# Kernel tuning notes

Measured on AMD Instinct MI355X. Metric: run time of the kernel, lower is better.

## Reference

```python
import jax, jax.numpy as jnp
import numpy as np

D_MODEL = 1024
D_FFN = 2048
N_EXPERTS = 8
TOP_K = 2
B, S = 2, 2048
LN_EPS = 1e-5


def setup_inputs() -> dict:
    key = jax.random.key(0)
    ks = jax.random.split(key, 6)
    scale = 0.02
    x = jax.random.normal(ks[0], (B, S, D_MODEL), dtype=jnp.float32)
    w_router = jax.random.normal(ks[1], (N_EXPERTS, D_MODEL), dtype=jnp.float32) * scale
    w_gate = jax.random.normal(ks[2], (N_EXPERTS, D_FFN, D_MODEL), dtype=jnp.float32) * scale
    w_up = jax.random.normal(ks[3], (N_EXPERTS, D_FFN, D_MODEL), dtype=jnp.float32) * scale
    w_down = jax.random.normal(ks[4], (N_EXPERTS, D_MODEL, D_FFN), dtype=jnp.float32) * scale
    ln_gamma = jnp.ones((D_MODEL,), dtype=jnp.float32)
    ln_beta = jnp.zeros((D_MODEL,), dtype=jnp.float32)
    return {"x": x, "w_router": w_router, "w_gate": w_gate, "w_up": w_up,
            "w_down": w_down, "ln_gamma": ln_gamma, "ln_beta": ln_beta}


def reference(x, w_router, w_gate, w_up, w_down, ln_gamma, ln_beta):
    # Router: top-k logits, softmax over selected k (matches MoERouter)
    logits = jnp.einsum('bsd,ed->bse', x, w_router)            # [B,S,E]
    top_vals, top_idx = jax.lax.top_k(logits, TOP_K)           # [B,S,k]
    rw = jax.nn.softmax(top_vals, axis=-1)                     # [B,S,k]

    # Dense per-expert SwiGLU over ALL tokens (faithful to the looped original:
    # sum over k of mask*weight*expert(x) == gather of per-expert outputs).
    gate = jnp.einsum('bsd,efd->ebsf', x, w_gate)              # [E,B,S,F]
    up = jnp.einsum('bsd,efd->ebsf', x, w_up)                  # [E,B,S,F]
    h = jax.nn.silu(gate) * up                                 # SwiGLU hidden
    y = jnp.einsum('ebsf,edf->bsed', h, w_down)                # [B,S,E,D]

    # Gather the k selected experts per token and combine with routing weights
    sel = jnp.take_along_axis(y, top_idx[..., None], axis=2)   # [B,S,k,D]
    out = jnp.sum(rw[..., None] * sel, axis=2)                 # [B,S,D]

    # LayerNorm (eps=1e-5, elementwise affine)
    mu = jnp.mean(out, axis=-1, keepdims=True)
    var = jnp.mean(jnp.square(out - mu), axis=-1, keepdims=True)
    out = (out - mu) * jax.lax.rsqrt(var + LN_EPS)
    return out * ln_gamma + ln_beta
```

## Files before the change

### kernel.cpp

```cpp
#include <hip/hip_runtime.h>


#define D_MODEL 1024
#define D_FFN   2048
#define N_EXP   8
#define TOKENS  4096
#define LISTCAP 4096
#define ROWS_PAD 8320
#define W_ELEM  16777216u

typedef __bf16 bf16x8 __attribute__((ext_vector_type(8)));
typedef float  f32x4  __attribute__((ext_vector_type(4)));

__device__ __forceinline__ ushort f2bf(float f) {
  union { float f; unsigned u; } v; v.f = f;
  unsigned u = v.u;
  u += 0x7fffu + ((u >> 16) & 1u);
  return (ushort)(u >> 16);
}
__device__ __forceinline__ float bf2f(ushort h) {
  union { unsigned u; float f; } v; v.u = ((unsigned)h) << 16; return v.f;
}
__device__ __forceinline__ void gl2lds16(const ushort* g, ushort* l) {
  __builtin_amdgcn_global_load_lds(
      (const __attribute__((address_space(1))) unsigned int*)g,
      (__attribute__((address_space(3))) unsigned int*)l, 16, 0, 0);
}


__global__ __launch_bounds__(256) void router_a_kernel(
    const float* __restrict__ x, const float* __restrict__ wr,
    ushort* __restrict__ xb, int* __restrict__ eids, float* __restrict__ wts)
{
  const int token = blockIdx.x * 4 + (threadIdx.x >> 6);
  const int lane  = threadIdx.x & 63;
  const float* xr = x + (size_t)token * D_MODEL + lane * 16;

  float xv[16];
  #pragma unroll
  for (int j = 0; j < 16; ++j) xv[j] = xr[j];

  ushort* xbr = xb + (size_t)token * D_MODEL + lane * 16;
  #pragma unroll
  for (int half = 0; half < 2; ++half) {
    ushort u8[8];
    #pragma unroll
    for (int j = 0; j < 8; ++j) u8[j] = f2bf(xv[half * 8 + j]);
    *(uint4*)(xbr + half * 8) = *(uint4*)u8;
  }

  float logit[N_EXP];
  #pragma unroll
  for (int e = 0; e < N_EXP; ++e) {
    const float* w = wr + e * D_MODEL + lane * 16;
    float p = 0.f;
    #pragma unroll
    for (int j = 0; j < 16; ++j) p += xv[j] * w[j];
    #pragma unroll
    for (int o = 32; o > 0; o >>= 1) p += __shfl_xor(p, o, 64);
    logit[e] = p;
  }

  if (lane == 0) {
    float v0 = -1e30f, v1 = -1e30f; int i0 = 0, i1 = 0;
    #pragma unroll
    for (int e = 0; e < N_EXP; ++e) {
      float v = logit[e];
      if (v > v0)      { v1 = v0; i1 = i0; v0 = v; i0 = e; }
      else if (v > v1) { v1 = v; i1 = e; }
    }
    float t  = expf(v1 - v0);
    eids[token] = i0 | (i1 << 8);
    wts[token * 2]     = 1.f / (1.f + t);
    wts[token * 2 + 1] = t   / (1.f + t);
  }
}

__global__ __launch_bounds__(1024) void build_lists_kernel(
    const int* __restrict__ eids, int* __restrict__ counts,
    int* __restrict__ tok_list, int* __restrict__ slots)
{
  const int e = blockIdx.x;
  const int t = threadIdx.x;

  int my_k[4];
  int c = 0;
  #pragma unroll
  for (int i = 0; i < 4; ++i) {
    int tok = t + i * 1024;
    int p  = eids[tok];
    int e0 = p & 0xff, e1 = (p >> 8) & 0xff;
    my_k[i] = (e0 == e) ? 0 : (e1 == e) ? 1 : -1;
    c += (my_k[i] >= 0) ? 1 : 0;
  }

  const int wave = t >> 6, lane = t & 63;
  int v = c;
  #pragma unroll
  for (int o = 1; o < 64; o <<= 1) {
    int n = __shfl_up(v, o, 64);
    if (lane >= o) v += n;
  }

  __shared__ int wsum[16];
  __shared__ int wbase[16];
  if (lane == 63) wsum[wave] = v;
  __syncthreads();
  if (t == 0) {
    int s = 0;
    #pragma unroll
    for (int w = 0; w < 16; ++w) { wbase[w] = s; s += wsum[w]; }
    counts[e] = s;
  }
  __syncthreads();

  int pos = wbase[wave] + v - c;
  #pragma unroll
  for (int i = 0; i < 4; ++i) {
    int tok = t + i * 1024;
    if (my_k[i] >= 0) {
      tok_list[e * LISTCAP + pos] = tok;
      slots[tok * 2 + my_k[i]] = e * LISTCAP + pos;
      pos++;
    }
  }
}

__global__ __launch_bounds__(256) void convert3_kernel(
    const float* __restrict__ wg, const float* __restrict__ wu,
    const float* __restrict__ wd, ushort* __restrict__ dstBase)
{
  const int bid = blockIdx.x;
  const int arr = bid >> 13;
  const float* src = (arr == 0) ? wg : (arr == 1) ? wu : wd;
  ushort* dst = dstBase + (size_t)arr * W_ELEM;
  const size_t base = (((size_t)(bid & 8191)) * 256 + threadIdx.x) * 8;
  float4 a = *(const float4*)(src + base);
  float4 b = *(const float4*)(src + base + 4);
  ushort u8[8] = {f2bf(a.x), f2bf(a.y), f2bf(a.z), f2bf(a.w),
                  f2bf(b.x), f2bf(b.y), f2bf(b.z), f2bf(b.w)};
  *(uint4*)(dst + base) = *(uint4*)u8;
}

__global__ __launch_bounds__(256, 3) void gateup3_kernel(
    const ushort* __restrict__ xb, const ushort* __restrict__ WgB,
    const ushort* __restrict__ WuB, const int* __restrict__ counts,
    const int* __restrict__ tok_list, ushort* __restrict__ H)
{
  const int e  = blockIdx.z;
  const int Ne = counts[e];
  const int m0 = blockIdx.y * 128;
  if (m0 >= Ne) return;
  const int n0 = blockIdx.x * 64;

  int rowoff = 0;
  for (int j = 0; j < e; ++j) rowoff += counts[j];

  __shared__ ushort As[128 * 64];
  __shared__ ushort Bg[64 * 64];
  __shared__ ushort Bu[64 * 64];
  __shared__ int tok_s[128];

  const int tid = threadIdx.x;
  if (tid < 128) {
    int i = m0 + tid;
    tok_s[tid] = tok_list[e * LISTCAP + (i < Ne ? i : Ne - 1)];
  }
  __syncthreads();

  const int wave = tid >> 6;
  const int lane = tid & 63;
  const int rsub = lane >> 3;
  const int cchk = lane & 7;
  const int co   = (cchk ^ rsub) << 3;

  const ushort* aSrc[4];
  #pragma unroll
  for (int i = 0; i < 4; ++i)
    aSrc[i] = xb + (size_t)tok_s[wave * 32 + i * 8 + rsub] * D_MODEL + co;
  const ushort* gS = WgB + ((size_t)e * D_FFN + n0 + wave * 16 + rsub) * D_MODEL + co;
  const ushort* uS = WuB + ((size_t)e * D_FFN + n0 + wave * 16 + rsub) * D_MODEL + co;
  ushort* aD = &As[(wave * 32) * 64];
  ushort* gD = &Bg[(wave * 16) * 64];
  ushort* uD = &Bu[(wave * 16) * 64];

  const int wm   = (wave >> 1) * 64;
  const int wn   = (wave & 1) * 32;
  const int lrow = lane & 15;
  const int lq   = lane >> 4;

  f32x4 accg[4][2], accu[4][2];
  #pragma unroll
  for (int i = 0; i < 4; ++i)
    #pragma unroll
    for (int j = 0; j < 2; ++j) {
      accg[i][j] = f32x4{0.f, 0.f, 0.f, 0.f};
      accu[i][j] = f32x4{0.f, 0.f, 0.f, 0.f};
    }

  for (int k0 = 0; k0 < D_MODEL; k0 += 64) {
    #pragma unroll
    for (int i = 0; i < 4; ++i) {
      gl2lds16(aSrc[i], aD + i * 8 * 64);
      aSrc[i] += 64;
    }
    #pragma unroll
    for (int i = 0; i < 2; ++i) {
      gl2lds16(gS + (size_t)i * 8 * D_MODEL, gD + i * 8 * 64);
      gl2lds16(uS + (size_t)i * 8 * D_MODEL, uD + i * 8 * 64);
    }
    gS += 64; uS += 64;
    __syncthreads();

    #pragma unroll
    for (int kk = 0; kk < 2; ++kk) {
      const int c = kk * 4 + lq;
      bf16x8 af[4], bgf[2], buf[2];
      #pragma unroll
      for (int mi = 0; mi < 4; ++mi) {
        int r = wm + mi * 16 + lrow;
        af[mi] = *(const bf16x8*)&As[r * 64 + ((c ^ (r & 7)) << 3)];
      }
      #pragma unroll
      for (int ni = 0; ni < 2; ++ni) {
        int r = wn + ni * 16 + lrow;
        int off = r * 64 + ((c ^ (r & 7)) << 3);
        bgf[ni] = *(const bf16x8*)&Bg[off];
        buf[ni] = *(const bf16x8*)&Bu[off];
      }
      #pragma unroll
      for (int mi = 0; mi < 4; ++mi)
        #pragma unroll
        for (int ni = 0; ni < 2; ++ni) {
          accg[mi][ni] = __builtin_amdgcn_mfma_f32_16x16x32_bf16(af[mi], bgf[ni], accg[mi][ni], 0, 0, 0);
          accu[mi][ni] = __builtin_amdgcn_mfma_f32_16x16x32_bf16(af[mi], buf[ni], accu[mi][ni], 0, 0, 0);
        }
    }
    __syncthreads();
  }

  const int rowbase = rowoff + m0;
  #pragma unroll
  for (int mi = 0; mi < 4; ++mi)
    #pragma unroll
    for (int r4 = 0; r4 < 4; ++r4) {
      int m = wm + mi * 16 + lq * 4 + r4;
      if (m0 + m < Ne) {
        ushort* hr = H + (size_t)(rowbase + m) * D_FFN + n0 + wn + lrow;
        #pragma unroll
        for (int ni = 0; ni < 2; ++ni) {
          float g = accg[mi][ni][r4];
          float u = accu[mi][ni][r4];
          float h = g / (1.f + __expf(-g)) * u;
          hr[ni * 16] = f2bf(h);
        }
      }
    }
}

__global__ __launch_bounds__(256, 3) void down3_kernel(
    const ushort* __restrict__ H, const ushort* __restrict__ WdB,
    const int* __restrict__ counts, ushort* __restrict__ Y)
{
  const int e  = blockIdx.z;
  const int Ne = counts[e];
  const int m0 = blockIdx.y * 128;
  if (m0 >= Ne) return;
  const int n0 = blockIdx.x * 128;

  int rowoff = 0;
  for (int j = 0; j < e; ++j) rowoff += counts[j];
  const int rowbase = rowoff + m0;

  __shared__ ushort As[128 * 64];
  __shared__ ushort Bd[128 * 64];

  const int tid  = threadIdx.x;
  const int wave = tid >> 6;
  const int lane = tid & 63;
  const int rsub = lane >> 3;
  const int cchk = lane & 7;
  const int co   = (cchk ^ rsub) << 3;

  const ushort* aS = H   + (size_t)(rowbase + wave * 32 + rsub) * D_FFN + co;
  const ushort* bS = WdB + (size_t)(e * D_MODEL + n0 + wave * 32 + rsub) * D_FFN + co;
  ushort* aD = &As[(wave * 32) * 64];
  ushort* bD = &Bd[(wave * 32) * 64];

  const int wm   = (wave >> 1) * 64;
  const int wn   = (wave & 1) * 64;
  const int lrow = lane & 15;
  const int lq   = lane >> 4;

  f32x4 acc[4][4];
  #pragma unroll
  for (int i = 0; i < 4; ++i)
    #pragma unroll
    for (int j = 0; j < 4; ++j) acc[i][j] = f32x4{0.f, 0.f, 0.f, 0.f};

  for (int k0 = 0; k0 < D_FFN; k0 += 64) {
    #pragma unroll
    for (int i = 0; i < 4; ++i) {
      gl2lds16(aS + (size_t)i * 8 * D_FFN, aD + i * 8 * 64);
      gl2lds16(bS + (size_t)i * 8 * D_FFN, bD + i * 8 * 64);
    }
    aS += 64; bS += 64;
    __syncthreads();

    #pragma unroll
    for (int kk = 0; kk < 2; ++kk) {
      const int c = kk * 4 + lq;
      bf16x8 af[4], bf[4];
      #pragma unroll
      for (int mi = 0; mi < 4; ++mi) {
        int r = wm + mi * 16 + lrow;
        af[mi] = *(const bf16x8*)&As[r * 64 + ((c ^ (r & 7)) << 3)];
      }
      #pragma unroll
      for (int ni = 0; ni < 4; ++ni) {
        int r = wn + ni * 16 + lrow;
        bf[ni] = *(const bf16x8*)&Bd[r * 64 + ((c ^ (r & 7)) << 3)];
      }
      #pragma unroll
      for (int mi = 0; mi < 4; ++mi)
        #pragma unroll
        for (int ni = 0; ni < 4; ++ni)
          acc[mi][ni] = __builtin_amdgcn_mfma_f32_16x16x32_bf16(af[mi], bf[ni], acc[mi][ni], 0, 0, 0);
    }
    __syncthreads();
  }

  #pragma unroll
  for (int mi = 0; mi < 4; ++mi)
    #pragma unroll
    for (int r4 = 0; r4 < 4; ++r4) {
      int m = wm + mi * 16 + lq * 4 + r4;
      if (m0 + m < Ne) {
        ushort* yr = Y + (size_t)(rowbase + m) * D_MODEL + n0 + wn + lrow;
        #pragma unroll
        for (int ni = 0; ni < 4; ++ni)
          yr[ni * 16] = f2bf(acc[mi][ni][r4]);
      }
    }
}

__global__ __launch_bounds__(256) void combine_ln3_kernel(
    const ushort* __restrict__ Y, const int* __restrict__ slots,
    const float* __restrict__ wts, const int* __restrict__ counts,
    const float* __restrict__ gamma, const float* __restrict__ beta,
    float* __restrict__ out)
{
  const int token = blockIdx.x;
  const int t = threadIdx.x;

  __shared__ int offs_s[N_EXP];
  if (t == 0) {
    int s = 0;
    #pragma unroll
    for (int j = 0; j < N_EXP; ++j) { offs_s[j] = s; s += counts[j]; }
  }
  __syncthreads();

  const int s0 = slots[token * 2], s1 = slots[token * 2 + 1];
  const float w0 = wts[token * 2], w1 = wts[token * 2 + 1];
  const int r0 = offs_s[s0 >> 12] + (s0 & (LISTCAP - 1));
  const int r1 = offs_s[s1 >> 12] + (s1 & (LISTCAP - 1));

  ushort4 a = *(const ushort4*)(Y + (size_t)r0 * D_MODEL + t * 4);
  ushort4 b = *(const ushort4*)(Y + (size_t)r1 * D_MODEL + t * 4);
  float4 v;
  v.x = w0 * bf2f(a.x) + w1 * bf2f(b.x);
  v.y = w0 * bf2f(a.y) + w1 * bf2f(b.y);
  v.z = w0 * bf2f(a.z) + w1 * bf2f(b.z);
  v.w = w0 * bf2f(a.w) + w1 * bf2f(b.w);

  float s = v.x + v.y + v.z + v.w;
  #pragma unroll
  for (int o = 32; o > 0; o >>= 1) s += __shfl_xor(s, o, 64);
  __shared__ float red[4];
  const int wave = t >> 6, lane = t & 63;
  if (lane == 0) red[wave] = s;
  __syncthreads();
  float mean = (red[0] + red[1] + red[2] + red[3]) * (1.f / D_MODEL);

  float dx = v.x - mean, dy = v.y - mean, dz = v.z - mean, dw = v.w - mean;
  float ss = dx * dx + dy * dy + dz * dz + dw * dw;
  #pragma unroll
  for (int o = 32; o > 0; o >>= 1) ss += __shfl_xor(ss, o, 64);
  __syncthreads();
  if (lane == 0) red[wave] = ss;
  __syncthreads();
  float var = (red[0] + red[1] + red[2] + red[3]) * (1.f / D_MODEL);
  float rs  = rsqrtf(var + 1e-5f);

  float4 g = ((const float4*)gamma)[t];
  float4 bb = ((const float4*)beta)[t];
  float4 o4;
  o4.x = dx * rs * g.x + bb.x;
  o4.y = dy * rs * g.y + bb.y;
  o4.z = dz * rs * g.z + bb.z;
  o4.w = dw * rs * g.w + bb.w;
  ((float4*)(out + (size_t)token * D_MODEL))[t] = o4;
}

__global__ __launch_bounds__(64) void router_kernel(
    const float* __restrict__ x, const float* __restrict__ wr,
    ushort* __restrict__ xb, int* __restrict__ counts,
    int* __restrict__ tok_list, float* __restrict__ wt_list)
{
  const int token = blockIdx.x;
  const int lane  = threadIdx.x;
  const float* xr = x + (size_t)token * D_MODEL;
  float xv[16];
  #pragma unroll
  for (int j = 0; j < 16; ++j) xv[j] = xr[j * 64 + lane];
  ushort* xbr = xb + (size_t)token * D_MODEL;
  #pragma unroll
  for (int j = 0; j < 16; ++j) xbr[j * 64 + lane] = f2bf(xv[j]);
  float logit[N_EXP];
  #pragma unroll
  for (int e = 0; e < N_EXP; ++e) {
    const float* w = wr + e * D_MODEL;
    float p = 0.f;
    #pragma unroll
    for (int j = 0; j < 16; ++j) p += xv[j] * w[j * 64 + lane];
    #pragma unroll
    for (int o = 32; o > 0; o >>= 1) p += __shfl_xor(p, o, 64);
    logit[e] = p;
  }
  if (lane == 0) {
    float v0 = -1e30f, v1 = -1e30f; int i0 = 0, i1 = 0;
    #pragma unroll
    for (int e = 0; e < N_EXP; ++e) {
      float v = logit[e];
      if (v > v0)      { v1 = v0; i1 = i0; v0 = v; i0 = e; }
      else if (v > v1) { v1 = v; i1 = e; }
    }
    float t  = expf(v1 - v0);
    float w0 = 1.f / (1.f + t);
    float w1 = t   / (1.f + t);
    int p0 = atomicAdd(&counts[i0], 1);
    tok_list[i0 * LISTCAP + p0] = token;
    wt_list[i0 * LISTCAP + p0] = w0;
    int p1 = atomicAdd(&counts[i1], 1);
    tok_list[i1 * LISTCAP + p1] = token;
    wt_list[i1 * LISTCAP + p1] = w1;
  }
}

__global__ void prefix_kernel(const int* __restrict__ counts, int* __restrict__ offsets)
{
  if (threadIdx.x == 0 && blockIdx.x == 0) {
    int s = 0;
    for (int e = 0; e < N_EXP; ++e) { offsets[e] = s; s += counts[e]; }
  }
}

__global__ __launch_bounds__(256, 2) void gateup_kernel(
    const ushort* __restrict__ xb, const float* __restrict__ wg,
    const float* __restrict__ wu, const int* __restrict__ counts,
    const int* __restrict__ offsets, const int* __restrict__ tok_list,
    ushort* __restrict__ H)
{
  const int e  = blockIdx.z;
  const int Ne = counts[e];
  const int m0 = blockIdx.y * 128;
  if (m0 >= Ne) return;
  const int n0 = blockIdx.x * 128;
  __shared__ ushort As[128][80];
  __shared__ ushort Bg[128][80];
  __shared__ ushort Bu[128][80];
  __shared__ int tok_s[128];
  const int tid = threadIdx.x;
  if (tid < 128) {
    int i = m0 + tid;
    tok_s[tid] = tok_list[e * LISTCAP + (i < Ne ? i : 0)];
  }
  __syncthreads();
  const int wave = tid >> 6;
  const int lane = tid & 63;
  const int wm   = (wave >> 1) * 64;
  const int wn   = (wave & 1) * 64;
  const int lrow = lane & 15;
  const int lk   = (lane >> 4) * 8;
  f32x4 accg[4][4], accu[4][4];
  #pragma unroll
  for (int i = 0; i < 4; ++i)
    #pragma unroll
    for (int j = 0; j < 4; ++j) {
      accg[i][j] = f32x4{0.f, 0.f, 0.f, 0.f};
      accu[i][j] = f32x4{0.f, 0.f, 0.f, 0.f};
    }
  const size_t wbase = ((size_t)e * D_FFN + n0) * D_MODEL;
  for (int k0 = 0; k0 < D_MODEL; k0 += 64) {
    #pragma unroll
    for (int r = 0; r < 4; ++r) {
      int idx = tid + r * 256;
      int row = idx >> 3;
      int c8  = (idx & 7) * 8;
      const ushort* src = xb + (size_t)tok_s[row] * D_MODEL + k0 + c8;
      *(uint4*)(&As[row][c8]) = *(const uint4*)src;
    }
    #pragma unroll
    for (int r = 0; r < 8; ++r) {
      int idx = tid + r * 256;
      int row = idx >> 4;
      int c4  = (idx & 15) * 4;
      const size_t off = wbase + (size_t)row * D_MODEL + k0 + c4;
      const float4 g = *(const float4*)(wg + off);
      const float4 u = *(const float4*)(wu + off);
      ushort4 gb; gb.x = f2bf(g.x); gb.y = f2bf(g.y); gb.z = f2bf(g.z); gb.w = f2bf(g.w);
      ushort4 ub; ub.x = f2bf(u.x); ub.y = f2bf(u.y); ub.z = f2bf(u.z); ub.w = f2bf(u.w);
      *(ushort4*)(&Bg[row][c4]) = gb;
      *(ushort4*)(&Bu[row][c4]) = ub;
    }
    __syncthreads();
    #pragma unroll
    for (int kk = 0; kk < 64; kk += 32) {
      bf16x8 af[4], bgf[4], buf[4];
      #pragma unroll
      for (int mi = 0; mi < 4; ++mi)
        af[mi] = *(const bf16x8*)(&As[wm + mi * 16 + lrow][kk + lk]);
      #pragma unroll
      for (int ni = 0; ni < 4; ++ni) {
        bgf[ni] = *(const bf16x8*)(&Bg[wn + ni * 16 + lrow][kk + lk]);
        buf[ni] = *(const bf16x8*)(&Bu[wn + ni * 16 + lrow][kk + lk]);
      }
      #pragma unroll
      for (int mi = 0; mi < 4; ++mi)
        #pragma unroll
        for (int ni = 0; ni < 4; ++ni) {
          accg[mi][ni] = __builtin_amdgcn_mfma_f32_16x16x32_bf16(af[mi], bgf[ni], accg[mi][ni], 0, 0, 0);
          accu[mi][ni] = __builtin_amdgcn_mfma_f32_16x16x32_bf16(af[mi], buf[ni], accu[mi][ni], 0, 0, 0);
        }
    }
    __syncthreads();
  }
  const int row_base = offsets[e] + m0;
  #pragma unroll
  for (int mi = 0; mi < 4; ++mi)
    #pragma unroll
    for (int ni = 0; ni < 4; ++ni)
      #pragma unroll
      for (int r4 = 0; r4 < 4; ++r4) {
        int m = wm + mi * 16 + (lane >> 4) * 4 + r4;
        if (m0 + m < Ne) {
          int n = wn + ni * 16 + (lane & 15);
          float g = accg[mi][ni][r4];
          float u = accu[mi][ni][r4];
          float h = g / (1.f + __expf(-g)) * u;
          H[(size_t)(row_base + m) * D_FFN + (n0 + n)] = f2bf(h);
        }
      }
}

__global__ __launch_bounds__(256, 2) void down_kernel(
    const ushort* __restrict__ H, const float* __restrict__ wd,
    const int* __restrict__ counts, const int* __restrict__ offsets,
    const int* __restrict__ tok_list, const float* __restrict__ wt_list,
    float* __restrict__ out)
{
  const int e  = blockIdx.z;
  const int Ne = counts[e];
  const int m0 = blockIdx.y * 128;
  if (m0 >= Ne) return;
  const int n0 = blockIdx.x * 128;
  __shared__ ushort As[128][80];
  __shared__ ushort Bd[128][80];
  __shared__ int   tok_s[128];
  __shared__ float wt_s[128];
  const int tid = threadIdx.x;
  if (tid < 128) {
    int i  = m0 + tid;
    int ok = (i < Ne);
    tok_s[tid] = tok_list[e * LISTCAP + (ok ? i : 0)];
    wt_s[tid]  = ok ? wt_list[e * LISTCAP + i] : 0.f;
  }
  __syncthreads();
  const int wave = tid >> 6;
  const int lane = tid & 63;
  const int wm   = (wave >> 1) * 64;
  const int wn   = (wave & 1) * 64;
  const int lrow = lane & 15;
  const int lk   = (lane >> 4) * 8;
  const int row_base = offsets[e] + m0;
  f32x4 acc[4][4];
  #pragma unroll
  for (int i = 0; i < 4; ++i)
    #pragma unroll
    for (int j = 0; j < 4; ++j) acc[i][j] = f32x4{0.f, 0.f, 0.f, 0.f};
  const size_t wdbase = ((size_t)e * D_MODEL + n0) * D_FFN;
  for (int k0 = 0; k0 < D_FFN; k0 += 64) {
    #pragma unroll
    for (int r = 0; r < 4; ++r) {
      int idx = tid + r * 256;
      int row = idx >> 3;
      int c8  = (idx & 7) * 8;
      const ushort* src = H + (size_t)(row_base + row) * D_FFN + k0 + c8;
      *(uint4*)(&As[row][c8]) = *(const uint4*)src;
    }
    #pragma unroll
    for (int r = 0; r < 8; ++r) {
      int idx = tid + r * 256;
      int row = idx >> 4;
      int c4  = (idx & 15) * 4;
      const float4 d = *(const float4*)(wd + wdbase + (size_t)row * D_FFN + k0 + c4);
      ushort4 db; db.x = f2bf(d.x); db.y = f2bf(d.y); db.z = f2bf(d.z); db.w = f2bf(d.w);
      *(ushort4*)(&Bd[row][c4]) = db;
    }
    __syncthreads();
    #pragma unroll
    for (int kk = 0; kk < 64; kk += 32) {
      bf16x8 af[4], bdf[4];
      #pragma unroll
      for (int mi = 0; mi < 4; ++mi)
        af[mi] = *(const bf16x8*)(&As[wm + mi * 16 + lrow][kk + lk]);
      #pragma unroll
      for (int ni = 0; ni < 4; ++ni)
        bdf[ni] = *(const bf16x8*)(&Bd[wn + ni * 16 + lrow][kk + lk]);
      #pragma unroll
      for (int mi = 0; mi < 4; ++mi)
        #pragma unroll
        for (int ni = 0; ni < 4; ++ni)
          acc[mi][ni] = __builtin_amdgcn_mfma_f32_16x16x32_bf16(af[mi], bdf[ni], acc[mi][ni], 0, 0, 0);
    }
    __syncthreads();
  }
  #pragma unroll
  for (int mi = 0; mi < 4; ++mi)
    #pragma unroll
    for (int ni = 0; ni < 4; ++ni)
      #pragma unroll
      for (int r4 = 0; r4 < 4; ++r4) {
        int m = wm + mi * 16 + (lane >> 4) * 4 + r4;
        if (m0 + m < Ne) {
          int n = wn + ni * 16 + (lane & 15);
          float v = acc[mi][ni][r4] * wt_s[m];
          atomicAdd(&out[(size_t)tok_s[m] * D_MODEL + (n0 + n)], v);
        }
      }
}

__global__ __launch_bounds__(256) void ln_kernel(
    float* __restrict__ out, const float* __restrict__ gamma,
    const float* __restrict__ beta)
{
  const int row = blockIdx.x;
  const int t   = threadIdx.x;
  float* rp = out + (size_t)row * D_MODEL;
  float4 v = ((const float4*)rp)[t];
  float s = v.x + v.y + v.z + v.w;
  #pragma unroll
  for (int o = 32; o > 0; o >>= 1) s += __shfl_xor(s, o, 64);
  __shared__ float red[4];
  const int wave = t >> 6, lane = t & 63;
  if (lane == 0) red[wave] = s;
  __syncthreads();
  float mean = (red[0] + red[1] + red[2] + red[3]) * (1.f / D_MODEL);
  float dx = v.x - mean, dy = v.y - mean, dz = v.z - mean, dw = v.w - mean;
  float ss = dx * dx + dy * dy + dz * dz + dw * dw;
  #pragma unroll
  for (int o = 32; o > 0; o >>= 1) ss += __shfl_xor(ss, o, 64);
  __syncthreads();
  if (lane == 0) red[wave] = ss;
  __syncthreads();
  float var = (red[0] + red[1] + red[2] + red[3]) * (1.f / D_MODEL);
  float rs  = rsqrtf(var + 1e-5f);
  float4 g = ((const float4*)gamma)[t];
  float4 b = ((const float4*)beta)[t];
  float4 o4;
  o4.x = dx * rs * g.x + b.x;
  o4.y = dy * rs * g.y + b.y;
  o4.z = dz * rs * g.z + b.z;
  o4.w = dw * rs * g.w + b.w;
  ((float4*)rp)[t] = o4;
}

extern "C" void kernel_launch(void* const* d_in, const int* in_sizes, int n_in,
                              void* d_out, int out_size, void* d_ws, size_t ws_size,
                              hipStream_t stream) {
  const float* x        = (const float*)d_in[0];
  const float* w_router = (const float*)d_in[1];
  const float* w_gate   = (const float*)d_in[2];
  const float* w_up     = (const float*)d_in[3];
  const float* w_down   = (const float*)d_in[4];
  const float* ln_gamma = (const float*)d_in[5];
  const float* ln_beta  = (const float*)d_in[6];
  float* out = (float*)d_out;
  char* ws = (char*)d_ws;

  const size_t META = 262144;
  const size_t NEED = META + 3 * (size_t)W_ELEM * 2
                      + (size_t)TOKENS * D_MODEL * 2
                      + (size_t)ROWS_PAD * D_FFN * 2;

  if (ws_size >= NEED) {
    int*   counts   = (int*)ws;
    int*   tok_list = (int*)(ws + 4096);
    int*   slots    = (int*)(ws + 4096 + 131072);
    float* wts      = (float*)(ws + 4096 + 131072 + 32768);
    int*   eids     = (int*)(ws + 4096 + 131072 + 32768 + 32768);
    ushort* WgB = (ushort*)(ws + META);
    ushort* WuB = WgB + W_ELEM;
    ushort* WdB = WuB + W_ELEM;
    ushort* xb  = WdB + W_ELEM;
    ushort* H   = xb + (size_t)TOKENS * D_MODEL;
    ushort* Y   = WgB;

    router_a_kernel<<<TOKENS / 4, 256, 0, stream>>>(x, w_router, xb, eids, wts);
    build_lists_kernel<<<N_EXP, 1024, 0, stream>>>(eids, counts, tok_list, slots);
    convert3_kernel<<<3 * 8192, 256, 0, stream>>>(w_gate, w_up, w_down, WgB);
    gateup3_kernel<<<dim3(D_FFN / 64, 32, N_EXP), 256, 0, stream>>>(
        xb, WgB, WuB, counts, tok_list, H);
    down3_kernel<<<dim3(D_MODEL / 128, 32, N_EXP), 256, 0, stream>>>(
        H, WdB, counts, Y);
    combine_ln3_kernel<<<TOKENS, 256, 0, stream>>>(Y, slots, wts, counts,
                                                   ln_gamma, ln_beta, out);
  } else {
    int*   counts   = (int*)ws;
    int*   offsets  = counts + 8;
    int*   tok_list = (int*)(ws + 256);
    float* wt_list  = (float*)(ws + 256 + LISTCAP * N_EXP * 4);
    ushort* xb      = (ushort*)(ws + 256 + LISTCAP * N_EXP * 8);
    ushort* H       = xb + (size_t)TOKENS * D_MODEL;

    hipMemsetAsync(counts, 0, 64, stream);
    hipMemsetAsync(out, 0, (size_t)TOKENS * D_MODEL * sizeof(float), stream);
    router_kernel<<<TOKENS, 64, 0, stream>>>(x, w_router, xb, counts, tok_list, wt_list);
    prefix_kernel<<<1, 64, 0, stream>>>(counts, offsets);
    gateup_kernel<<<dim3(D_FFN / 128, 32, N_EXP), 256, 0, stream>>>(
        xb, w_gate, w_up, counts, offsets, tok_list, H);
    down_kernel<<<dim3(D_MODEL / 128, 32, N_EXP), 256, 0, stream>>>(
        H, w_down, counts, offsets, tok_list, wt_list, out);
    ln_kernel<<<TOKENS, 256, 0, stream>>>(out, ln_gamma, ln_beta);
  }
}
```

Measured before the change: 378.1 us.

## Fuse fp32-to-bf16 weight conversion into grouped GEMM tile loads

Removes the separate pass that converts all expert weights to bf16. The gate/up and down GEMM kernels now read fp32 weights directly, convert them with packed bf16 instructions, and write the results into swizzled shared memory. This saves a full read and write of the weights, but each weight tile is now fetched and converted once per M-tile block, at twice the byte width. The loads also go through registers instead of direct global-to-LDS transfers, which can stall the load path. Y also gets its own workspace region instead of reusing the converted-weight buffer.

Result: slower. 475.5 us (+25.7%).

```diff
diff --git a/kernel.cpp b/kernel.cpp
--- a/kernel.cpp
+++ b/kernel.cpp
@@ -7,7 +7,6 @@
 #define TOKENS  4096
 #define LISTCAP 4096
 #define ROWS_PAD 8320
-#define W_ELEM  16777216u
 
 typedef __bf16 bf16x8 __attribute__((ext_vector_type(8)));
 typedef float  f32x4  __attribute__((ext_vector_type(4)));
@@ -25,6 +24,11 @@
   __builtin_amdgcn_global_load_lds(
       (const __attribute__((address_space(1))) unsigned int*)g,
       (__attribute__((address_space(3))) unsigned int*)l, 16, 0, 0);
+}
+__device__ __forceinline__ unsigned cvtpk(float lo, float hi) {
+  unsigned r;
+  asm("v_cvt_pk_bf16_f32 %0, %1, %2" : "=v"(r) : "v"(lo), "v"(hi));
+  return r;
 }
 
 
@@ -126,25 +130,9 @@
   }
 }
 
-__global__ __launch_bounds__(256) void convert3_kernel(
-    const float* __restrict__ wg, const float* __restrict__ wu,
-    const float* __restrict__ wd, ushort* __restrict__ dstBase)
-{
-  const int bid = blockIdx.x;
-  const int arr = bid >> 13;
-  const float* src = (arr == 0) ? wg : (arr == 1) ? wu : wd;
-  ushort* dst = dstBase + (size_t)arr * W_ELEM;
-  const size_t base = (((size_t)(bid & 8191)) * 256 + threadIdx.x) * 8;
-  float4 a = *(const float4*)(src + base);
-  float4 b = *(const float4*)(src + base + 4);
-  ushort u8[8] = {f2bf(a.x), f2bf(a.y), f2bf(a.z), f2bf(a.w),
-                  f2bf(b.x), f2bf(b.y), f2bf(b.z), f2bf(b.w)};
-  *(uint4*)(dst + base) = *(uint4*)u8;
-}
-
 __global__ __launch_bounds__(256, 3) void gateup3_kernel(
-    const ushort* __restrict__ xb, const ushort* __restrict__ WgB,
-    const ushort* __restrict__ WuB, const int* __restrict__ counts,
+    const ushort* __restrict__ xb, const float* __restrict__ wg,
+    const float* __restrict__ wu, const int* __restrict__ counts,
     const int* __restrict__ tok_list, ushort* __restrict__ H)
 {
   const int e  = blockIdx.z;
@@ -178,11 +166,17 @@
   #pragma unroll
   for (int i = 0; i < 4; ++i)
     aSrc[i] = xb + (size_t)tok_s[wave * 32 + i * 8 + rsub] * D_MODEL + co;
-  const ushort* gS = WgB + ((size_t)e * D_FFN + n0 + wave * 16 + rsub) * D_MODEL + co;
-  const ushort* uS = WuB + ((size_t)e * D_FFN + n0 + wave * 16 + rsub) * D_MODEL + co;
   ushort* aD = &As[(wave * 32) * 64];
-  ushort* gD = &Bg[(wave * 16) * 64];
-  ushort* uD = &Bu[(wave * 16) * 64];
+
+  const int br  = tid >> 2;
+  const int bc  = (tid & 3) * 16;
+  const int c8a = (tid & 3) * 2;
+  const float* gF = wg + ((size_t)e * D_FFN + n0 + br) * D_MODEL + bc;
+  const float* uF = wu + ((size_t)e * D_FFN + n0 + br) * D_MODEL + bc;
+  ushort* gW0 = &Bg[br * 64 + (((c8a    ) ^ (br & 7)) << 3)];
+  ushort* gW1 = &Bg[br * 64 + (((c8a + 1) ^ (br & 7)) << 3)];
+  ushort* uW0 = &Bu[br * 64 + (((c8a    ) ^ (br & 7)) << 3)];
+  ushort* uW1 = &Bu[br * 64 + (((c8a + 1) ^ (br & 7)) << 3)];
 
   const int wm   = (wave >> 1) * 64;
   const int wn   = (wave & 1) * 32;
@@ -204,12 +198,28 @@
       gl2lds16(aSrc[i], aD + i * 8 * 64);
       aSrc[i] += 64;
     }
-    #pragma unroll
-    for (int i = 0; i < 2; ++i) {
-      gl2lds16(gS + (size_t)i * 8 * D_MODEL, gD + i * 8 * 64);
-      gl2lds16(uS + (size_t)i * 8 * D_MODEL, uD + i * 8 * 64);
-    }
-    gS += 64; uS += 64;
+    float4 g0 = *(const float4*)(gF);
+    float4 g1 = *(const float4*)(gF + 4);
+    float4 g2 = *(const float4*)(gF + 8);
+    float4 g3 = *(const float4*)(gF + 12);
+    float4 u0 = *(const float4*)(uF);
+    float4 u1 = *(const float4*)(uF + 4);
+    float4 u2 = *(const float4*)(uF + 8);
+    float4 u3 = *(const float4*)(uF + 12);
+    gF += 64; uF += 64;
+    uint4 q;
+    q.x = cvtpk(g0.x, g0.y); q.y = cvtpk(g0.z, g0.w);
+    q.z = cvtpk(g1.x, g1.y); q.w = cvtpk(g1.z, g1.w);
+    *(uint4*)gW0 = q;
+    q.x = cvtpk(g2.x, g2.y); q.y = cvtpk(g2.z, g2.w);
+    q.z = cvtpk(g3.x, g3.y); q.w = cvtpk(g3.z, g3.w);
+    *(uint4*)gW1 = q;
+    q.x = cvtpk(u0.x, u0.y); q.y = cvtpk(u0.z, u0.w);
+    q.z = cvtpk(u1.x, u1.y); q.w = cvtpk(u1.z, u1.w);
+    *(uint4*)uW0 = q;
+    q.x = cvtpk(u2.x, u2.y); q.y = cvtpk(u2.z, u2.w);
+    q.z = cvtpk(u3.x, u3.y); q.w = cvtpk(u3.z, u3.w);
+    *(uint4*)uW1 = q;
     __syncthreads();
 
     #pragma unroll
@@ -259,7 +269,7 @@
 }
 
 __global__ __launch_bounds__(256, 3) void down3_kernel(
-    const ushort* __restrict__ H, const ushort* __restrict__ WdB,
+    const ushort* __restrict__ H, const float* __restrict__ wd,
     const int* __restrict__ counts, ushort* __restrict__ Y)
 {
   const int e  = blockIdx.z;
@@ -282,10 +292,17 @@
   const int cchk = lane & 7;
   const int co   = (cchk ^ rsub) << 3;
 
-  const ushort* aS = H   + (size_t)(rowbase + wave * 32 + rsub) * D_FFN + co;
-  const ushort* bS = WdB + (size_t)(e * D_MODEL + n0 + wave * 32 + rsub) * D_FFN + co;
+  const ushort* aS = H + (size_t)(rowbase + wave * 32 + rsub) * D_FFN + co;
   ushort* aD = &As[(wave * 32) * 64];
-  ushort* bD = &Bd[(wave * 32) * 64];
+
+  const int br  = tid >> 1;
+  const int bc  = (tid & 1) * 32;
+  const int c8a = (tid & 1) * 4;
+  const float* dF = wd + ((size_t)e * D_MODEL + n0 + br) * D_FFN + bc;
+  ushort* dW0 = &Bd[br * 64 + (((c8a    ) ^ (br & 7)) << 3)];
+  ushort* dW1 = &Bd[br * 64 + (((c8a + 1) ^ (br & 7)) << 3)];
+  ushort* dW2 = &Bd[br * 64 + (((c8a + 2) ^ (br & 7)) << 3)];
+  ushort* dW3 = &Bd[br * 64 + (((c8a + 3) ^ (br & 7)) << 3)];
 
   const int wm   = (wave >> 1) * 64;
   const int wn   = (wave & 1) * 64;
@@ -300,11 +317,32 @@
 
   for (int k0 = 0; k0 < D_FFN; k0 += 64) {
     #pragma unroll
-    for (int i = 0; i < 4; ++i) {
+    for (int i = 0; i < 4; ++i)
       gl2lds16(aS + (size_t)i * 8 * D_FFN, aD + i * 8 * 64);
-      gl2lds16(bS + (size_t)i * 8 * D_FFN, bD + i * 8 * 64);
-    }
-    aS += 64; bS += 64;
+    aS += 64;
+
+    float4 d0 = *(const float4*)(dF);
+    float4 d1 = *(const float4*)(dF + 4);
+    float4 d2 = *(const float4*)(dF + 8);
+    float4 d3 = *(const float4*)(dF + 12);
+    float4 d4 = *(const float4*)(dF + 16);
+    float4 d5 = *(const float4*)(dF + 20);
+    float4 d6 = *(const float4*)(dF + 24);
+    float4 d7 = *(const float4*)(dF + 28);
+    dF += 64;
+    uint4 q;
+    q.x = cvtpk(d0.x, d0.y); q.y = cvtpk(d0.z, d0.w);
+    q.z = cvtpk(d1.x, d1.y); q.w = cvtpk(d1.z, d1.w);
+    *(uint4*)dW0 = q;
+    q.x = cvtpk(d2.x, d2.y); q.y = cvtpk(d2.z, d2.w);
+    q.z = cvtpk(d3.x, d3.y); q.w = cvtpk(d3.z, d3.w);
+    *(uint4*)dW1 = q;
+    q.x = cvtpk(d4.x, d4.y); q.y = cvtpk(d4.z, d4.w);
+    q.z = cvtpk(d5.x, d5.y); q.w = cvtpk(d5.z, d5.w);
+    *(uint4*)dW2 = q;
+    q.x = cvtpk(d6.x, d6.y); q.y = cvtpk(d6.z, d6.w);
+    q.z = cvtpk(d7.x, d7.y); q.w = cvtpk(d7.z, d7.w);
+    *(uint4*)dW3 = q;
     __syncthreads();
 
     #pragma unroll
@@ -690,9 +728,9 @@
   char* ws = (char*)d_ws;
 
   const size_t META = 262144;
-  const size_t NEED = META + 3 * (size_t)W_ELEM * 2
-                      + (size_t)TOKENS * D_MODEL * 2
-                      + (size_t)ROWS_PAD * D_FFN * 2;
+  const size_t NEED = META + (size_t)TOKENS * D_MODEL * 2
+                      + (size_t)ROWS_PAD * D_FFN * 2
+                      + (size_t)ROWS_PAD * D_MODEL * 2;
 
   if (ws_size >= NEED) {
     int*   counts   = (int*)ws;
@@ -700,20 +738,16 @@
     int*   slots    = (int*)(ws + 4096 + 131072);
     float* wts      = (float*)(ws + 4096 + 131072 + 32768);
     int*   eids     = (int*)(ws + 4096 + 131072 + 32768 + 32768);
-    ushort* WgB = (ushort*)(ws + META);
-    ushort* WuB = WgB + W_ELEM;
-    ushort* WdB = WuB + W_ELEM;
-    ushort* xb  = WdB + W_ELEM;
-    ushort* H   = xb + (size_t)TOKENS * D_MODEL;
-    ushort* Y   = WgB;
+    ushort* xb = (ushort*)(ws + META);
+    ushort* H  = xb + (size_t)TOKENS * D_MODEL;
+    ushort* Y  = H + (size_t)ROWS_PAD * D_FFN;
 
     router_a_kernel<<<TOKENS / 4, 256, 0, stream>>>(x, w_router, xb, eids, wts);
     build_lists_kernel<<<N_EXP, 1024, 0, stream>>>(eids, counts, tok_list, slots);
-    convert3_kernel<<<3 * 8192, 256, 0, stream>>>(w_gate, w_up, w_down, WgB);
     gateup3_kernel<<<dim3(D_FFN / 64, 32, N_EXP), 256, 0, stream>>>(
-        xb, WgB, WuB, counts, tok_list, H);
+        xb, w_gate, w_up, counts, tok_list, H);
     down3_kernel<<<dim3(D_MODEL / 128, 32, N_EXP), 256, 0, stream>>>(
-        H, WdB, counts, Y);
+        H, w_down, counts, Y);
     combine_ln3_kernel<<<TOKENS, 256, 0, stream>>>(Y, slots, wts, counts,
                                                    ln_gamma, ln_beta, out);
   } else {
```
